# Kernel tuning notes

Hardware: AMD Instinct MI355X
Metric: run time of the kernel (lower is better)

The kernel has to match this reference:

```python
import jax, jax.numpy as jnp
import numpy as np

TEMPERATURE = 0.07
ASYM_F = 1.5
ASYM_M = 0.5
N_F, N_M, D = 8192, 8192, 128


def setup_inputs() -> dict:
    key = jax.random.key(0)
    kf, km = jax.random.split(key)
    proj_f = jax.random.normal(kf, (N_F, D), dtype=jnp.float32)
    proj_m = jax.random.normal(km, (N_M, D), dtype=jnp.float32)
    # module expects L2-normalized projections
    proj_f = proj_f / jnp.linalg.norm(proj_f, axis=1, keepdims=True)
    proj_m = proj_m / jnp.linalg.norm(proj_m, axis=1, keepdims=True)
    return {"proj_f": proj_f, "proj_m": proj_m}


def _directional_loss(anchor, pos, temperature):
    # anchor: (Na, D), pos: (Np, D)
    sim_pos = jnp.einsum('ad,pd->ap', anchor, pos) / temperature        # (Na, Np)
    sim_neg = jnp.einsum('ad,bd->ab', anchor, anchor) / temperature    # (Na, Na)
    n = anchor.shape[0]
    eye = jnp.eye(n, dtype=bool)
    sim_neg = jnp.where(eye, -jnp.inf, sim_neg)  # mask self-similarity
    numerator = jax.nn.logsumexp(sim_pos, axis=1)
    # logsumexp over concat([sim_pos, sim_neg]) == logaddexp of row lses (no concat materialized)
    denominator = jnp.logaddexp(numerator, jax.nn.logsumexp(sim_neg, axis=1))
    return -jnp.mean(numerator - denominator)


def reference(proj_f, proj_m):
    loss_f2m = _directional_loss(proj_f, proj_m, TEMPERATURE)
    loss_m2f = _directional_loss(proj_m, proj_f, TEMPERATURE)
    return ASYM_F * loss_f2m + ASYM_M * loss_m2f
```

## Files before the change

### kernel.cpp

```cpp
#include <hip/hip_runtime.h>

#define NROWS 8192
#define KD    128
#define K1C   20.6099291260f

typedef __bf16 bf16x8 __attribute__((ext_vector_type(8)));
typedef float  f32x16 __attribute__((ext_vector_type(16)));

typedef __attribute__((address_space(1))) void* gas_ptr;
typedef __attribute__((address_space(3))) void* las_ptr;

__device__ __forceinline__ unsigned short f2bf(float x) {
  unsigned int u = __builtin_bit_cast(unsigned int, x);
  unsigned int r = (u + 0x7FFFu + ((u >> 16) & 1u)) >> 16;
  return (unsigned short)r;
}

__global__ __launch_bounds__(256) void prep_kernel(const float4* __restrict__ F4,
                                                   const float4* __restrict__ M4,
                                                   ushort4* __restrict__ Fb4,
                                                   ushort4* __restrict__ Mb4,
                                                   float* __restrict__ sums) {
  int i = blockIdx.x * 256 + threadIdx.x;
  float4 f = F4[i];
  float4 m = M4[i];
  ushort4 fo, mo;
  fo.x = f2bf(f.x); fo.y = f2bf(f.y); fo.z = f2bf(f.z); fo.w = f2bf(f.w);
  mo.x = f2bf(m.x); mo.y = f2bf(m.y); mo.z = f2bf(m.z); mo.w = f2bf(m.w);
  Fb4[i] = fo;
  Mb4[i] = mo;
  if (i < 4 * NROWS) sums[i] = 0.0f;
}

__global__ __launch_bounds__(512, 4) void gemm_kernel(const unsigned short* __restrict__ Fb,
                                                      const unsigned short* __restrict__ Mb,
                                                      float* __restrict__ sums) {
  __shared__ __align__(16) unsigned short lds[2][128 * 128];

  const int bx = blockIdx.x;
  const int by = blockIdx.y;
  const int z  = blockIdx.z;

  const unsigned short* A;
  const unsigned short* B;
  float* rowsum;
  float* colsum = nullptr;
  if (z == 0)      { A = Fb; B = Mb; rowsum = sums;             colsum = sums + NROWS; }
  else if (z == 1) { A = Fb; B = Fb; rowsum = sums + 2 * NROWS; }
  else             { A = Mb; B = Mb; rowsum = sums + 3 * NROWS; }

  const int tid  = threadIdx.x;
  const int lane = tid & 63;
  const int wave = tid >> 6;
  const int wr = wave >> 1;
  const int wc = wave & 1;
  const int l31 = lane & 31, lh = lane >> 5;

  const int srow = tid >> 4;
  const int soff = srow * 256 + ((((tid & 15) * 16)) ^ ((srow & 7) << 4));

#define STAGE(dstbuf, src) do {                                                          \
    const char* s_ = (const char*)(src) + soff;                                          \
    char* d_ = (char*)(dstbuf) + tid * 16;                                               \
    __builtin_amdgcn_global_load_lds((gas_ptr)(s_),         (las_ptr)(d_),         16, 0, 0); \
    __builtin_amdgcn_global_load_lds((gas_ptr)(s_ + 8192),  (las_ptr)(d_ + 8192),  16, 0, 0); \
    __builtin_amdgcn_global_load_lds((gas_ptr)(s_ + 16384), (las_ptr)(d_ + 16384), 16, 0, 0); \
    __builtin_amdgcn_global_load_lds((gas_ptr)(s_ + 24576), (las_ptr)(d_ + 24576), 16, 0, 0); \
  } while (0)

  const unsigned short* Abase = A + (size_t)by * 128 * KD;
  const unsigned short* Bbase = B + (size_t)bx * 1024 * KD;

  STAGE(lds[0], Abase);
  STAGE(lds[1], Bbase);
  __syncthreads();

  bf16x8 afrag[8];
  {
    const int arow = wr * 32 + l31;
    const char* ab = (const char*)lds[0] + arow * 256;
    const int sw = (arow & 7) << 4;
    #pragma unroll
    for (int ks = 0; ks < 8; ++ks)
      afrag[ks] = *(const bf16x8*)(ab + ((ks * 32 + lh * 16) ^ sw));
  }

  float rowacc[16];
  #pragma unroll
  for (int i = 0; i < 16; ++i) rowacc[i] = 0.f;

  __syncthreads();

  const int brow = wc * 64 + l31;
  const int bsw  = (brow & 7) << 4;

  for (int t = 0; t < 8; ++t) {
    if (t < 7) STAGE(lds[t & 1], Bbase + (size_t)(t + 1) * 128 * KD);

    const char* bb = (const char*)lds[(t + 1) & 1];
    const char* bb0 = bb + brow * 256;
    const char* bb1 = bb0 + 32 * 256;

    f32x16 acc0 = {}, acc1 = {};
    #pragma unroll
    for (int ks = 0; ks < 8; ++ks) {
      const int c = (ks * 32 + lh * 16);
      bf16x8 b0 = *(const bf16x8*)(bb0 + (c ^ bsw));
      bf16x8 b1 = *(const bf16x8*)(bb1 + (c ^ bsw));
      acc0 = __builtin_amdgcn_mfma_f32_32x32x16_bf16(afrag[ks], b0, acc0, 0, 0, 0);
      acc1 = __builtin_amdgcn_mfma_f32_32x32x16_bf16(afrag[ks], b1, acc1, 0, 0, 0);
    }

    const bool diag = (z > 0) && (bx * 8 + t == by);
    if (z == 0) {
      float col0 = 0.f, col1 = 0.f;
      #pragma unroll
      for (int r = 0; r < 16; ++r) {
        float v0 = __builtin_amdgcn_exp2f(acc0[r] * K1C - K1C);
        float v1 = __builtin_amdgcn_exp2f(acc1[r] * K1C - K1C);
        rowacc[r] += v0 + v1;
        col0 += v0; col1 += v1;
      }
      col0 += __shfl_xor(col0, 32);
      col1 += __shfl_xor(col1, 32);
      if (lh == 0) {
        float* cp = colsum + bx * 1024 + t * 128 + wc * 64 + l31;
        unsafeAtomicAdd(cp, col0);
        unsafeAtomicAdd(cp + 32, col1);
      }
    } else {
      #pragma unroll
      for (int r = 0; r < 16; ++r) {
        float v0 = __builtin_amdgcn_exp2f(acc0[r] * K1C - K1C);
        float v1 = __builtin_amdgcn_exp2f(acc1[r] * K1C - K1C);
        if (diag) {
          const int lr = wr * 32 + (r & 3) + 8 * (r >> 2) + 4 * lh;
          const int lc = wc * 64 + l31;
          if (lr == lc)      v0 = 0.f;
          if (lr == lc + 32) v1 = 0.f;
        }
        rowacc[r] += v0 + v1;
      }
    }
    __syncthreads();
  }

  #pragma unroll
  for (int i = 0; i < 16; ++i) {
    float v = rowacc[i];
    v += __shfl_xor(v, 1);
    v += __shfl_xor(v, 2);
    v += __shfl_xor(v, 4);
    v += __shfl_xor(v, 8);
    v += __shfl_xor(v, 16);
    rowacc[i] = v;
  }
  if (l31 == 0) {
    const int rbase = by * 128 + wr * 32 + 4 * lh;
    #pragma unroll
    for (int i = 0; i < 16; ++i)
      unsafeAtomicAdd(rowsum + rbase + (i & 3) + 8 * (i >> 2), rowacc[i]);
  }
#undef STAGE
}

__global__ __launch_bounds__(1024) void loss_kernel(const float* __restrict__ sums,
                                                    float* __restrict__ out) {
  const float* Spf = sums;
  const float* Spm = sums + NROWS;
  const float* Snf = sums + 2 * NROWS;
  const float* Snm = sums + 3 * NROWS;
  float accf = 0.f, accm = 0.f;
  for (int i = threadIdx.x; i < NROWS; i += 1024) {
    accf += log1pf(Snf[i] / Spf[i]);
    accm += log1pf(Snm[i] / Spm[i]);
  }
  float v = 1.5f * accf + 0.5f * accm;
  #pragma unroll
  for (int s = 1; s < 64; s <<= 1) v += __shfl_xor(v, s);
  __shared__ float red[16];
  if ((threadIdx.x & 63) == 0) red[threadIdx.x >> 6] = v;
  __syncthreads();
  if (threadIdx.x == 0) {
    float s = 0.f;
    #pragma unroll
    for (int i = 0; i < 16; ++i) s += red[i];
    out[0] = s * (1.0f / NROWS);
  }
}

extern "C" void kernel_launch(void* const* d_in, const int* in_sizes, int n_in,
                              void* d_out, int out_size, void* d_ws, size_t ws_size,
                              hipStream_t stream) {
  (void)in_sizes; (void)n_in; (void)out_size; (void)ws_size;
  const float* F = (const float*)d_in[0];
  const float* M = (const float*)d_in[1];
  float* out = (float*)d_out;

  float* sums = (float*)d_ws;
  unsigned short* Fb = (unsigned short*)((char*)d_ws + 4 * NROWS * sizeof(float));
  unsigned short* Mb = Fb + (size_t)NROWS * KD;

  prep_kernel<<<dim3(NROWS * KD / 4 / 256), dim3(256), 0, stream>>>(
      (const float4*)F, (const float4*)M, (ushort4*)Fb, (ushort4*)Mb, sums);
  gemm_kernel<<<dim3(8, 64, 3), dim3(512), 0, stream>>>(Fb, Mb, sums);
  loss_kernel<<<dim3(1), dim3(1024), 0, stream>>>(sums, out);
}
```

Measured before the change: 100.5 us.

## Split GEMM kernels, enlarge per-wave tiles, fold temperature scale into bf16 inputs

The prep kernel now multiplies both inputs by sqrt(K1C) before the bf16 conversion. That lets the GEMM epilogue call exp2 on the accumulator directly, dropping the per-element FMA. The offset this removes scales every row sum by the same factor, so the sum ratios the loss reads are unaffected. The single three-way GEMM becomes a cross kernel (row and column sums, no diagonal logic) and a symmetric kernel with diagonal masking. Both use 256-thread blocks where each wave computes a 64x64 tile, so A and B fragments are reused across more MFMAs. The symmetric kernel double-buffers its accumulators to overlap each tile's exp epilogue with the next tile's MFMAs, and both raise wave priority around the MFMA block. In exchange there are fewer waves per CU, higher register pressure and an extra kernel launch.

```diff
diff --git a/kernel.cpp b/kernel.cpp
--- a/kernel.cpp
+++ b/kernel.cpp
@@ -2,7 +2,7 @@
 
 #define NROWS 8192
 #define KD    128
-#define K1C   20.6099291260f
+#define SQK1C 4.5398163f
 
 typedef __bf16 bf16x8 __attribute__((ext_vector_type(8)));
 typedef float  f32x16 __attribute__((ext_vector_type(16)));
@@ -25,143 +25,238 @@
   float4 f = F4[i];
   float4 m = M4[i];
   ushort4 fo, mo;
-  fo.x = f2bf(f.x); fo.y = f2bf(f.y); fo.z = f2bf(f.z); fo.w = f2bf(f.w);
-  mo.x = f2bf(m.x); mo.y = f2bf(m.y); mo.z = f2bf(m.z); mo.w = f2bf(m.w);
+  fo.x = f2bf(f.x * SQK1C); fo.y = f2bf(f.y * SQK1C);
+  fo.z = f2bf(f.z * SQK1C); fo.w = f2bf(f.w * SQK1C);
+  mo.x = f2bf(m.x * SQK1C); mo.y = f2bf(m.y * SQK1C);
+  mo.z = f2bf(m.z * SQK1C); mo.w = f2bf(m.w * SQK1C);
   Fb4[i] = fo;
   Mb4[i] = mo;
   if (i < 4 * NROWS) sums[i] = 0.0f;
 }
 
-__global__ __launch_bounds__(512, 4) void gemm_kernel(const unsigned short* __restrict__ Fb,
-                                                      const unsigned short* __restrict__ Mb,
-                                                      float* __restrict__ sums) {
+__global__ __launch_bounds__(256, 2) void gemm_fm(const unsigned short* __restrict__ Fb,
+                                                  const unsigned short* __restrict__ Mb,
+                                                  float* __restrict__ sums) {
   __shared__ __align__(16) unsigned short lds[2][128 * 128];
-
   const int bx = blockIdx.x;
   const int by = blockIdx.y;
-  const int z  = blockIdx.z;
-
-  const unsigned short* A;
-  const unsigned short* B;
-  float* rowsum;
-  float* colsum = nullptr;
-  if (z == 0)      { A = Fb; B = Mb; rowsum = sums;             colsum = sums + NROWS; }
-  else if (z == 1) { A = Fb; B = Fb; rowsum = sums + 2 * NROWS; }
-  else             { A = Mb; B = Mb; rowsum = sums + 3 * NROWS; }
-
-  const int tid  = threadIdx.x;
-  const int lane = tid & 63;
-  const int wave = tid >> 6;
-  const int wr = wave >> 1;
-  const int wc = wave & 1;
+  const int tid = threadIdx.x, lane = tid & 63, wave = tid >> 6;
+  const int wr = wave >> 1, wc = wave & 1;
   const int l31 = lane & 31, lh = lane >> 5;
-
-  const int srow = tid >> 4;
-  const int soff = srow * 256 + ((((tid & 15) * 16)) ^ ((srow & 7) << 4));
-
-#define STAGE(dstbuf, src) do {                                                          \
-    const char* s_ = (const char*)(src) + soff;                                          \
-    char* d_ = (char*)(dstbuf) + tid * 16;                                               \
-    __builtin_amdgcn_global_load_lds((gas_ptr)(s_),         (las_ptr)(d_),         16, 0, 0); \
-    __builtin_amdgcn_global_load_lds((gas_ptr)(s_ + 8192),  (las_ptr)(d_ + 8192),  16, 0, 0); \
-    __builtin_amdgcn_global_load_lds((gas_ptr)(s_ + 16384), (las_ptr)(d_ + 16384), 16, 0, 0); \
-    __builtin_amdgcn_global_load_lds((gas_ptr)(s_ + 24576), (las_ptr)(d_ + 24576), 16, 0, 0); \
-  } while (0)
-
-  const unsigned short* Abase = A + (size_t)by * 128 * KD;
-  const unsigned short* Bbase = B + (size_t)bx * 1024 * KD;
-
-  STAGE(lds[0], Abase);
-  STAGE(lds[1], Bbase);
-  __syncthreads();
-
-  bf16x8 afrag[8];
-  {
-    const int arow = wr * 32 + l31;
-    const char* ab = (const char*)lds[0] + arow * 256;
-    const int sw = (arow & 7) << 4;
+  float* rowsum = sums;
+  float* colsum = sums + NROWS;
+
+  auto stage = [&](void* dst, const unsigned short* src) {
+    #pragma unroll
+    for (int i = 0; i < 8; ++i) {
+      const int lin = tid * 16 + i * 4096;
+      const int row = lin >> 8;
+      const int sbc = (lin & 255) ^ ((row & 7) << 4);
+      __builtin_amdgcn_global_load_lds((gas_ptr)((const char*)src + row * 256 + sbc),
+                                       (las_ptr)((char*)dst + lin), 16, 0, 0);
+    }
+  };
+
+  stage(lds[0], Fb + (size_t)by * 128 * KD);
+  stage(lds[1], Mb + (size_t)bx * 1024 * KD);
+  __syncthreads();
+
+  bf16x8 af[2][8];
+  #pragma unroll
+  for (int mb = 0; mb < 2; ++mb) {
+    const int row = wr * 64 + mb * 32 + l31;
+    const char* ab = (const char*)lds[0] + row * 256;
+    const int sw = (row & 7) << 4;
     #pragma unroll
     for (int ks = 0; ks < 8; ++ks)
-      afrag[ks] = *(const bf16x8*)(ab + ((ks * 32 + lh * 16) ^ sw));
-  }
-
-  float rowacc[16];
-  #pragma unroll
-  for (int i = 0; i < 16; ++i) rowacc[i] = 0.f;
-
-  __syncthreads();
-
-  const int brow = wc * 64 + l31;
-  const int bsw  = (brow & 7) << 4;
-
+      af[mb][ks] = *(const bf16x8*)(ab + ((ks * 32 + lh * 16) ^ sw));
+  }
+  __syncthreads();
+
+  float rowacc[32];
+  #pragma unroll
+  for (int i = 0; i < 32; ++i) rowacc[i] = 0.f;
+
+  const unsigned short* Bbase = Mb + (size_t)bx * 1024 * KD;
+  const int prow0 = wc * 64 + l31;
+  const int psw = (prow0 & 7) << 4;
+
+  #pragma unroll
   for (int t = 0; t < 8; ++t) {
-    if (t < 7) STAGE(lds[t & 1], Bbase + (size_t)(t + 1) * 128 * KD);
-
+    if (t < 7) stage(lds[t & 1], Bbase + (size_t)(t + 1) * 128 * KD);
     const char* bb = (const char*)lds[(t + 1) & 1];
-    const char* bb0 = bb + brow * 256;
-    const char* bb1 = bb0 + 32 * 256;
-
-    f32x16 acc0 = {}, acc1 = {};
-    #pragma unroll
-    for (int ks = 0; ks < 8; ++ks) {
-      const int c = (ks * 32 + lh * 16);
-      bf16x8 b0 = *(const bf16x8*)(bb0 + (c ^ bsw));
-      bf16x8 b1 = *(const bf16x8*)(bb1 + (c ^ bsw));
-      acc0 = __builtin_amdgcn_mfma_f32_32x32x16_bf16(afrag[ks], b0, acc0, 0, 0, 0);
-      acc1 = __builtin_amdgcn_mfma_f32_32x32x16_bf16(afrag[ks], b1, acc1, 0, 0, 0);
-    }
-
-    const bool diag = (z > 0) && (bx * 8 + t == by);
-    if (z == 0) {
-      float col0 = 0.f, col1 = 0.f;
+    f32x16 acc[2][2];
+    __builtin_amdgcn_s_setprio(1);
+    #pragma unroll
+    for (int nb = 0; nb < 2; ++nb) {
+      const char* pb = bb + (prow0 + nb * 32) * 256;
+      bf16x8 bp[8];
+      #pragma unroll
+      for (int ks = 0; ks < 8; ++ks)
+        bp[ks] = *(const bf16x8*)(pb + ((ks * 32 + lh * 16) ^ psw));
+      #pragma unroll
+      for (int ks = 0; ks < 8; ++ks) {
+        acc[0][nb] = __builtin_amdgcn_mfma_f32_32x32x16_bf16(af[0][ks], bp[ks],
+                        ks ? acc[0][nb] : (f32x16){}, 0, 0, 0);
+        acc[1][nb] = __builtin_amdgcn_mfma_f32_32x32x16_bf16(af[1][ks], bp[ks],
+                        ks ? acc[1][nb] : (f32x16){}, 0, 0, 0);
+      }
+    }
+    __builtin_amdgcn_s_setprio(0);
+
+    float ca0 = 0.f, ca1 = 0.f;
+    #pragma unroll
+    for (int mb = 0; mb < 2; ++mb) {
       #pragma unroll
       for (int r = 0; r < 16; ++r) {
-        float v0 = __builtin_amdgcn_exp2f(acc0[r] * K1C - K1C);
-        float v1 = __builtin_amdgcn_exp2f(acc1[r] * K1C - K1C);
-        rowacc[r] += v0 + v1;
-        col0 += v0; col1 += v1;
+        float v0 = __builtin_amdgcn_exp2f(acc[mb][0][r]);
+        float v1 = __builtin_amdgcn_exp2f(acc[mb][1][r]);
+        rowacc[mb * 16 + r] += v0 + v1;
+        ca0 += v0; ca1 += v1;
       }
-      col0 += __shfl_xor(col0, 32);
-      col1 += __shfl_xor(col1, 32);
-      if (lh == 0) {
-        float* cp = colsum + bx * 1024 + t * 128 + wc * 64 + l31;
-        unsafeAtomicAdd(cp, col0);
-        unsafeAtomicAdd(cp + 32, col1);
-      }
-    } else {
-      #pragma unroll
-      for (int r = 0; r < 16; ++r) {
-        float v0 = __builtin_amdgcn_exp2f(acc0[r] * K1C - K1C);
-        float v1 = __builtin_amdgcn_exp2f(acc1[r] * K1C - K1C);
-        if (diag) {
-          const int lr = wr * 32 + (r & 3) + 8 * (r >> 2) + 4 * lh;
-          const int lc = wc * 64 + l31;
-          if (lr == lc)      v0 = 0.f;
-          if (lr == lc + 32) v1 = 0.f;
-        }
-        rowacc[r] += v0 + v1;
-      }
+    }
+    ca0 += __shfl_xor(ca0, 32);
+    ca1 += __shfl_xor(ca1, 32);
+    if (lh == 0) {
+      float* cp = colsum + bx * 1024 + t * 128 + wc * 64 + l31;
+      unsafeAtomicAdd(cp, ca0);
+      unsafeAtomicAdd(cp + 32, ca1);
     }
     __syncthreads();
   }
 
   #pragma unroll
-  for (int i = 0; i < 16; ++i) {
+  for (int i = 0; i < 32; ++i) {
     float v = rowacc[i];
     v += __shfl_xor(v, 1);
     v += __shfl_xor(v, 2);
     v += __shfl_xor(v, 4);
     v += __shfl_xor(v, 8);
     v += __shfl_xor(v, 16);
-    rowacc[i] = v;
-  }
-  if (l31 == 0) {
-    const int rbase = by * 128 + wr * 32 + 4 * lh;
-    #pragma unroll
-    for (int i = 0; i < 16; ++i)
-      unsafeAtomicAdd(rowsum + rbase + (i & 3) + 8 * (i >> 2), rowacc[i]);
-  }
-#undef STAGE
+    if (l31 == 0) {
+      const int r = i & 15, mb = i >> 4;
+      unsafeAtomicAdd(rowsum + by * 128 + wr * 64 + mb * 32 +
+                          (r & 3) + 8 * (r >> 2) + 4 * lh, v);
+    }
+  }
+}
+
+__global__ __launch_bounds__(256, 2) void gemm_sym(const unsigned short* __restrict__ Fb,
+                                                   const unsigned short* __restrict__ Mb,
+                                                   float* __restrict__ sums) {
+  __shared__ __align__(16) unsigned short lds[2][128 * 128];
+  const int bx = blockIdx.x, by = blockIdx.y;
+  const unsigned short* X = blockIdx.z ? Mb : Fb;
+  float* rowsum = sums + (blockIdx.z ? 3 : 2) * NROWS;
+
+  const int tid = threadIdx.x, lane = tid & 63, wave = tid >> 6;
+  const int wr = wave >> 1, wc = wave & 1;
+  const int l31 = lane & 31, lh = lane >> 5;
+
+  auto stage = [&](void* dst, const unsigned short* src) {
+    #pragma unroll
+    for (int i = 0; i < 8; ++i) {
+      const int lin = tid * 16 + i * 4096;
+      const int row = lin >> 8;
+      const int sbc = (lin & 255) ^ ((row & 7) << 4);
+      __builtin_amdgcn_global_load_lds((gas_ptr)((const char*)src + row * 256 + sbc),
+                                       (las_ptr)((char*)dst + lin), 16, 0, 0);
+    }
+  };
+
+  stage(lds[0], X + (size_t)by * 128 * KD);
+  stage(lds[1], X + (size_t)bx * 1024 * KD);
+  __syncthreads();
+
+  bf16x8 af[2][8];
+  #pragma unroll
+  for (int jb = 0; jb < 2; ++jb) {
+    const int row = wr * 64 + jb * 32 + l31;
+    const char* ab = (const char*)lds[0] + row * 256;
+    const int sw = (row & 7) << 4;
+    #pragma unroll
+    for (int ks = 0; ks < 8; ++ks)
+      af[jb][ks] = *(const bf16x8*)(ab + ((ks * 32 + lh * 16) ^ sw));
+  }
+  __syncthreads();
+
+  float ra0 = 0.f, ra1 = 0.f;
+  const unsigned short* Bbase = X + (size_t)bx * 1024 * KD;
+  const int prow0 = wc * 64 + l31;
+  const int psw = (prow0 & 7) << 4;
+  const int Rb0 = by * 128 + wr * 64;
+  const int pat = (0 & 3);
+
+  f32x16 acc[2][2][2];
+
+  auto epi = [&](int tp, f32x16 (&ac)[2][2]) {
+    const int Cb0 = bx * 1024 + tp * 128 + wc * 64;
+    #pragma unroll
+    for (int jb = 0; jb < 2; ++jb) {
+      const int Rb = Rb0 + jb * 32;
+      float s = 0.f;
+      #pragma unroll
+      for (int ib = 0; ib < 2; ++ib) {
+        const bool dg = (Rb == Cb0 + ib * 32);
+        float p[4];
+        #pragma unroll
+        for (int q = 0; q < 4; ++q) {
+          float v0 = __builtin_amdgcn_exp2f(ac[jb][ib][q * 4 + 0]);
+          float v1 = __builtin_amdgcn_exp2f(ac[jb][ib][q * 4 + 1]);
+          float v2 = __builtin_amdgcn_exp2f(ac[jb][ib][q * 4 + 2]);
+          float v3 = __builtin_amdgcn_exp2f(ac[jb][ib][q * 4 + 3]);
+          if (dg) {
+            #pragma unroll
+            for (int j = 0; j < 4; ++j) {
+              if ((j + 8 * q + 4 * lh) == l31) {
+                if (j == 0) v0 = 0.f;
+                if (j == 1) v1 = 0.f;
+                if (j == 2) v2 = 0.f;
+                if (j == 3) v3 = 0.f;
+              }
+            }
+          }
+          p[q] = (v0 + v1) + (v2 + v3);
+        }
+        s += (p[0] + p[1]) + (p[2] + p[3]);
+      }
+      if (jb == 0) ra0 += s; else ra1 += s;
+    }
+  };
+
+  #pragma unroll
+  for (int t = 0; t < 8; ++t) {
+    if (t < 7) stage(lds[t & 1], Bbase + (size_t)(t + 1) * 128 * KD);
+    const char* bb = (const char*)lds[(t + 1) & 1];
+    __builtin_amdgcn_s_setprio(1);
+    #pragma unroll
+    for (int ib = 0; ib < 2; ++ib) {
+      const char* pb = bb + (prow0 + ib * 32) * 256;
+      bf16x8 bp[8];
+      #pragma unroll
+      for (int ks = 0; ks < 8; ++ks)
+        bp[ks] = *(const bf16x8*)(pb + ((ks * 32 + lh * 16) ^ psw));
+      #pragma unroll
+      for (int ks = 0; ks < 8; ++ks) {
+        acc[t & 1][0][ib] = __builtin_amdgcn_mfma_f32_32x32x16_bf16(bp[ks], af[0][ks],
+                               ks ? acc[t & 1][0][ib] : (f32x16){}, 0, 0, 0);
+        acc[t & 1][1][ib] = __builtin_amdgcn_mfma_f32_32x32x16_bf16(bp[ks], af[1][ks],
+                               ks ? acc[t & 1][1][ib] : (f32x16){}, 0, 0, 0);
+      }
+    }
+    __builtin_amdgcn_s_setprio(0);
+    if (t > 0) epi(t - 1, acc[(t - 1) & 1]);
+    __syncthreads();
+  }
+  epi(7, acc[1]);
+
+  ra0 += __shfl_xor(ra0, 32);
+  ra1 += __shfl_xor(ra1, 32);
+  if (lh == 0) {
+    unsafeAtomicAdd(rowsum + Rb0 + l31, ra0);
+    unsafeAtomicAdd(rowsum + Rb0 + 32 + l31, ra1);
+  }
+  (void)pat;
 }
 
 __global__ __launch_bounds__(1024) void loss_kernel(const float* __restrict__ sums,
@@ -203,6 +298,7 @@
 
   prep_kernel<<<dim3(NROWS * KD / 4 / 256), dim3(256), 0, stream>>>(
       (const float4*)F, (const float4*)M, (ushort4*)Fb, (ushort4*)Mb, sums);
-  gemm_kernel<<<dim3(8, 64, 3), dim3(512), 0, stream>>>(Fb, Mb, sums);
+  gemm_fm<<<dim3(8, 64), dim3(256), 0, stream>>>(Fb, Mb, sums);
+  gemm_sym<<<dim3(8, 64, 2), dim3(256), 0, stream>>>(Fb, Mb, sums);
   loss_kernel<<<dim3(1), dim3(1024), 0, stream>>>(sums, out);
 }
```

New measurement: 271.6 us. +170.3%, slower.
